# Performance work log

Hardware: AMD Instinct MI355X
Metric: run time of the kernel (lower is better)

The kernel has to match this reference:

```python
import jax, jax.numpy as jnp
import numpy as np

N_TRIPLES = 100_000    # number of (head, rel, attr) triples
TOTAL_CHARS = 1_600_000  # total characters across all attribute strings (~16/triple)
CHAR_VOCAB = 10_000
N_ENT = 100_000
D = 128                # embedding dim shared by char and entity tables


def setup_inputs() -> dict:
    key = jax.random.key(0)
    k1, k2, k3, k4, k5 = jax.random.split(key, 5)
    char_embeddings = jax.random.normal(k1, (CHAR_VOCAB, D), dtype=jnp.float32)
    entity_embeddings = jax.random.normal(k2, (N_ENT, D), dtype=jnp.float32)
    head_ids = jax.random.randint(k3, (N_TRIPLES,), 0, N_ENT, dtype=jnp.int32)
    char_ids = jax.random.randint(k4, (TOTAL_CHARS,), 0, CHAR_VOCAB, dtype=jnp.int32)
    # sorted segment ids emulate the per-triple ragged grouping (offsets form)
    segment_ids = jnp.sort(jax.random.randint(k5, (TOTAL_CHARS,), 0, N_TRIPLES, dtype=jnp.int32))
    return {
        "char_embeddings": char_embeddings,
        "entity_embeddings": entity_embeddings,
        "head_ids": head_ids,
        "char_ids": char_ids,
        "segment_ids": segment_ids,
    }


def reference(char_embeddings, entity_embeddings, head_ids, char_ids, segment_ids):
    n = head_ids.shape[0]
    # ragged embedding-bag: gather char rows, sum within each triple's segment
    t = jax.ops.segment_sum(char_embeddings[char_ids], segment_ids, num_segments=n)  # [N, D]
    h = entity_embeddings[head_ids]  # [N, D]
    # torch.norm with no dim = global Frobenius norm (faithful to original)
    h = h / jnp.linalg.norm(h)
    t = t / jnp.linalg.norm(t)
    return jnp.sum(1.0 - jnp.sum(h * t, axis=1))
```

## Files before the change

### kernel.cpp

```cpp
#include <hip/hip_runtime.h>

#define DIM   128
#define HALF  64
#define CPT   256
#define TAIL  64
#define WPB   4

__global__ __launch_bounds__(256) void fused_kernel(
    const float* __restrict__ char_emb,
    const float* __restrict__ ent,
    const int* __restrict__ head_ids,
    const int* __restrict__ char_ids,
    const int* __restrict__ seg_ids,
    float* __restrict__ pb,
    int total_chars, int n_triples, int hh_per_block)
{
    __shared__ __align__(16) int s_off[WPB][CPT + TAIL];
    __shared__ int s_sid[WPB][CPT + TAIL];
    __shared__ float r_scr[3][WPB];

    const int tid  = threadIdx.x;
    const int lane = tid & 63;
    const int wid  = tid >> 6;
    const int colb = lane << 2;

    float ht = 0.f, tt = 0.f, hh = 0.f;

    const int slice = blockIdx.x & 1;
    const int sco   = slice << 8;
    const int chunk = (blockIdx.x >> 1) * WPB + wid;
    const int start = chunk * CPT;
    const int len   = min(CPT, total_chars - start);
    const int sl    = min(CPT + TAIL, total_chars - start);
    const char* cb  = (const char*)char_emb;
    const float* ee = ent + slice * HALF + lane;

    for (int c = lane; c < sl; c += 64) {
        s_off[wid][c] = (char_ids[start + c] << 9) + sco;
        s_sid[wid][c] = seg_ids[start + c];
    }
    unsigned long long mk[4] = {0ull, 0ull, 0ull, 0ull};
    if (len == CPT) {
#pragma unroll
        for (int grp = 0; grp < 4; ++grp) {
            const int c = start + grp * 64 + lane;
            const int s1 = seg_ids[c];
            const int s0 = (c > 0) ? seg_ids[c - 1] : (s1 + 1);
            mk[grp] = __ballot(s1 != s0);
        }
    }
    __syncthreads();

    if (len == CPT) {
        int cur = __builtin_amdgcn_readfirstlane(s_sid[wid][0]);
        float hv = ee[(size_t)head_ids[cur] * DIM];
        float acc = 0.f;
        bool live = false;
        float vA[16], vB[16];

#define PF(BUF, B) { \
    _Pragma("unroll") \
    for (int q = 0; q < 4; ++q) { \
        const int4 o4 = *(const int4*)&s_off[wid][(B) * 16 + q * 4]; \
        BUF[q * 4 + 0] = *(const float*)(cb + (size_t)(unsigned)(o4.x + colb)); \
        BUF[q * 4 + 1] = *(const float*)(cb + (size_t)(unsigned)(o4.y + colb)); \
        BUF[q * 4 + 2] = *(const float*)(cb + (size_t)(unsigned)(o4.z + colb)); \
        BUF[q * 4 + 3] = *(const float*)(cb + (size_t)(unsigned)(o4.w + colb)); \
    } }

#define CS(BUF, B) { \
    _Pragma("unroll") \
    for (int j = 0; j < 16; ++j) { \
        if (mk[(B) >> 2] & (1ull << (((B) & 3) * 16 + j))) {    \
            if (live) { ht = fmaf(hv, acc, ht); tt = fmaf(acc, acc, tt); } \
            live = true; \
            acc = 0.f; \
            cur = __builtin_amdgcn_readfirstlane(s_sid[wid][(B) * 16 + j]); \
            hv = ee[(size_t)head_ids[cur] * DIM];     \
        } \
        acc += BUF[j]; \
    } }

        PF(vA, 0)
#pragma unroll
        for (int B = 0; B < 16; ++B) {
            if (B + 1 < 16) { if (B & 1) { PF(vA, B + 1) } else { PF(vB, B + 1) } }
            if (B & 1) { CS(vB, B) } else { CS(vA, B) }
        }

        if (live) {
            int e = CPT;
            bool ended = false;
            while (e < sl) {
                const int idx = e + lane;
                const bool differ = (idx < sl) && (s_sid[wid][idx] != cur);
                const unsigned long long bm = __ballot(differ);
                const int run = bm ? (__ffsll((long long)bm) - 1)
                                   : min(64, sl - e);
                for (int j = 0; j < run; j += 4) {
                    const int mm2 = min(4, run - j);
                    float vv[4];
#pragma unroll
                    for (int k = 0; k < 4; ++k) {
                        if (k < mm2)
                            vv[k] = *(const float*)(cb +
                                (size_t)(unsigned)(s_off[wid][e + j + k] + colb));
                    }
                    for (int k = 0; k < mm2; ++k) acc += vv[k];
                }
                e += run;
                if (bm) { ended = true; break; }
            }
            if (!ended && start + sl < total_chars) {
                int gg = start + sl;
                while (gg < total_chars && seg_ids[gg] == cur) {
                    acc += *(const float*)(cb +
                        (size_t)(unsigned)((char_ids[gg] << 9) + sco + colb));
                    ++gg;
                }
            }
            ht = fmaf(hv, acc, ht);
            tt = fmaf(acc, acc, tt);
        }
    } else if (len > 0) {
        const float* cembF = char_emb + slice * HALF + lane;
        int p = 0;
        if (start > 0) {
            const int prev = seg_ids[start - 1];
            while (p < len && seg_ids[start + p] == prev) ++p;
        }
        if (p < len) {
            int cur = seg_ids[start + p];
            float acc = 0.f;
            float hv = ee[(size_t)head_ids[cur] * DIM];
            for (int c = p; c < len; ++c) {
                const int sid = seg_ids[start + c];
                if (sid != cur) {
                    ht += hv * acc; tt += acc * acc;
                    acc = 0.f; cur = sid;
                    hv = ee[(size_t)head_ids[cur] * DIM];
                }
                acc += cembF[(size_t)char_ids[start + c] * DIM];
            }
            int gg = start + len;
            while (gg < total_chars && seg_ids[gg] == cur) {
                acc += cembF[(size_t)char_ids[gg] * DIM];
                ++gg;
            }
            ht += hv * acc; tt += acc * acc;
        }
    }

    {
        const float4* e4 = (const float4*)ent;
        const long base = (long)blockIdx.x * hh_per_block * 32;
        const long lim  = (long)n_triples * 32;
        for (int s = tid; s < hh_per_block * 32; s += 256) {
            const long f = base + s;
            if (f < lim) {
                const int row = (int)(f >> 5);
                const int hid = head_ids[row];
                const float4 v = e4[(size_t)hid * 32 + (int)(f & 31)];
                hh += v.x * v.x + v.y * v.y + v.z * v.z + v.w * v.w;
            }
        }
    }

#pragma unroll
    for (int off = 32; off > 0; off >>= 1) {
        ht += __shfl_down(ht, off);
        tt += __shfl_down(tt, off);
        hh += __shfl_down(hh, off);
    }
    if (lane == 0) { r_scr[0][wid] = ht; r_scr[1][wid] = tt; r_scr[2][wid] = hh; }
    __syncthreads();
    if (tid == 0) {
        float a = 0.f, b = 0.f, c = 0.f;
#pragma unroll
        for (int w = 0; w < WPB; ++w) {
            a += r_scr[0][w]; b += r_scr[1][w]; c += r_scr[2][w];
        }
        pb[blockIdx.x * 3 + 0] = a;
        pb[blockIdx.x * 3 + 1] = b;
        pb[blockIdx.x * 3 + 2] = c;
    }
}

__global__ __launch_bounds__(256) void reduce_kernel(
    const float* __restrict__ pb, int nb, float* __restrict__ out,
    int n_triples)
{
    double ht = 0.0, tt = 0.0, hh = 0.0;
    for (int i = threadIdx.x; i < nb; i += 256) {
        ht += (double)pb[i * 3 + 0];
        tt += (double)pb[i * 3 + 1];
        hh += (double)pb[i * 3 + 2];
    }
#pragma unroll
    for (int off = 32; off > 0; off >>= 1) {
        ht += __shfl_down(ht, off);
        tt += __shfl_down(tt, off);
        hh += __shfl_down(hh, off);
    }
    __shared__ double sd[3][4];
    const int wid = threadIdx.x >> 6;
    if ((threadIdx.x & 63) == 0) { sd[0][wid] = ht; sd[1][wid] = tt; sd[2][wid] = hh; }
    __syncthreads();
    if (threadIdx.x == 0) {
        double a = 0.0, b = 0.0, c = 0.0;
        for (int w = 0; w < 4; ++w) { a += sd[0][w]; b += sd[1][w]; c += sd[2][w]; }
        out[0] = (float)((double)n_triples - a / sqrt(c * b));
    }
}

extern "C" void kernel_launch(void* const* d_in, const int* in_sizes, int n_in,
                              void* d_out, int out_size, void* d_ws, size_t ws_size,
                              hipStream_t stream)
{
    const float* char_emb = (const float*)d_in[0];
    const float* ent_emb  = (const float*)d_in[1];
    const int* head_ids   = (const int*)d_in[2];
    const int* char_ids   = (const int*)d_in[3];
    const int* seg_ids    = (const int*)d_in[4];
    const int n_triples   = in_sizes[2];
    const int total_chars = in_sizes[3];

    const int n_chunks = (total_chars + CPT - 1) / CPT;
    const int bps = (n_chunks + WPB - 1) / WPB;
    const int nsb = 2 * bps;
    const int hhpb = (n_triples + nsb - 1) / nsb;

    float* pb = (float*)d_ws;

    fused_kernel<<<nsb, 256, 0, stream>>>(char_emb, ent_emb, head_ids,
                                          char_ids, seg_ids, pb,
                                          total_chars, n_triples, hhpb);
    reduce_kernel<<<1, 256, 0, stream>>>(pb, nsb, (float*)d_out, n_triples);
}
```

Before: 165.4 us.

## Process full embedding row per wave with float2 loads and prefetched head ids

```diff
diff --git a/kernel.cpp b/kernel.cpp
--- a/kernel.cpp
+++ b/kernel.cpp
@@ -1,10 +1,10 @@
 #include <hip/hip_runtime.h>
 
 #define DIM   128
-#define HALF  64
 #define CPT   256
 #define TAIL  64
 #define WPB   4
+#define QD    40
 
 __global__ __launch_bounds__(256) void fused_kernel(
     const float* __restrict__ char_emb,
@@ -17,68 +17,83 @@
 {
     __shared__ __align__(16) int s_off[WPB][CPT + TAIL];
     __shared__ int s_sid[WPB][CPT + TAIL];
+    __shared__ int s_hq[WPB][QD];
     __shared__ float r_scr[3][WPB];
 
     const int tid  = threadIdx.x;
     const int lane = tid & 63;
     const int wid  = tid >> 6;
-    const int colb = lane << 2;
+    const int colb = lane << 3;
 
     float ht = 0.f, tt = 0.f, hh = 0.f;
 
-    const int slice = blockIdx.x & 1;
-    const int sco   = slice << 8;
-    const int chunk = (blockIdx.x >> 1) * WPB + wid;
+    const int chunk = blockIdx.x * WPB + wid;
     const int start = chunk * CPT;
     const int len   = min(CPT, total_chars - start);
     const int sl    = min(CPT + TAIL, total_chars - start);
     const char* cb  = (const char*)char_emb;
-    const float* ee = ent + slice * HALF + lane;
+    const float* ee = ent + (lane << 1);
 
     for (int c = lane; c < sl; c += 64) {
-        s_off[wid][c] = (char_ids[start + c] << 9) + sco;
+        s_off[wid][c] = char_ids[start + c] << 9;
         s_sid[wid][c] = seg_ids[start + c];
     }
+
     unsigned long long mk[4] = {0ull, 0ull, 0ull, 0ull};
     if (len == CPT) {
+        int rbase = 0;
 #pragma unroll
         for (int grp = 0; grp < 4; ++grp) {
-            const int c = start + grp * 64 + lane;
-            const int s1 = seg_ids[c];
-            const int s0 = (c > 0) ? seg_ids[c - 1] : (s1 + 1);
-            mk[grp] = __ballot(s1 != s0);
+            const int cc = grp * 64 + lane;
+            const int s1 = s_sid[wid][cc];
+            const int ip = (cc > 0) ? cc - 1 : 0;
+            int s0 = s_sid[wid][ip];
+            if (cc == 0) s0 = (start > 0) ? seg_ids[start - 1] : s1 + 1;
+            const bool bnd = (s1 != s0);
+            mk[grp] = __ballot(bnd);
+            const int rk = rbase + (int)__popcll(mk[grp] & ((1ull << lane) - 1ull));
+            if (bnd && rk < QD) s_hq[wid][rk] = head_ids[s1];
+            rbase += (int)__popcll(mk[grp]);
         }
     }
     __syncthreads();
 
     if (len == CPT) {
-        int cur = __builtin_amdgcn_readfirstlane(s_sid[wid][0]);
-        float hv = ee[(size_t)head_ids[cur] * DIM];
-        float acc = 0.f;
+        int cur = 0;
+        float2 hv;  hv.x = 0.f;  hv.y = 0.f;
+        float2 acc; acc.x = 0.f; acc.y = 0.f;
         bool live = false;
-        float vA[16], vB[16];
+        int rk = 0;
+        int nhid = __builtin_amdgcn_readfirstlane(s_hq[wid][0]);
+        float2 vA[16], vB[16];
 
 #define PF(BUF, B) { \
     _Pragma("unroll") \
     for (int q = 0; q < 4; ++q) { \
         const int4 o4 = *(const int4*)&s_off[wid][(B) * 16 + q * 4]; \
-        BUF[q * 4 + 0] = *(const float*)(cb + (size_t)(unsigned)(o4.x + colb)); \
-        BUF[q * 4 + 1] = *(const float*)(cb + (size_t)(unsigned)(o4.y + colb)); \
-        BUF[q * 4 + 2] = *(const float*)(cb + (size_t)(unsigned)(o4.z + colb)); \
-        BUF[q * 4 + 3] = *(const float*)(cb + (size_t)(unsigned)(o4.w + colb)); \
+        BUF[q * 4 + 0] = *(const float2*)(cb + (size_t)(unsigned)(o4.x + colb)); \
+        BUF[q * 4 + 1] = *(const float2*)(cb + (size_t)(unsigned)(o4.y + colb)); \
+        BUF[q * 4 + 2] = *(const float2*)(cb + (size_t)(unsigned)(o4.z + colb)); \
+        BUF[q * 4 + 3] = *(const float2*)(cb + (size_t)(unsigned)(o4.w + colb)); \
     } }
 
 #define CS(BUF, B) { \
     _Pragma("unroll") \
     for (int j = 0; j < 16; ++j) { \
         if (mk[(B) >> 2] & (1ull << (((B) & 3) * 16 + j))) {    \
-            if (live) { ht = fmaf(hv, acc, ht); tt = fmaf(acc, acc, tt); } \
+            if (live) { \
+                ht = fmaf(hv.x, acc.x, ht); ht = fmaf(hv.y, acc.y, ht); \
+                tt = fmaf(acc.x, acc.x, tt); tt = fmaf(acc.y, acc.y, tt); \
+            } \
             live = true; \
-            acc = 0.f; \
+            acc.x = 0.f; acc.y = 0.f; \
             cur = __builtin_amdgcn_readfirstlane(s_sid[wid][(B) * 16 + j]); \
-            hv = ee[(size_t)head_ids[cur] * DIM];     \
+            const int hid = (rk < QD) ? nhid : head_ids[cur];   \
+            hv = *(const float2*)(ee + (size_t)hid * DIM); \
+            ++rk; \
+            nhid = __builtin_amdgcn_readfirstlane(s_hq[wid][rk < QD ? rk : QD - 1]); \
         } \
-        acc += BUF[j]; \
+        acc.x += BUF[j].x; acc.y += BUF[j].y; \
     } }
 
         PF(vA, 0)
@@ -99,14 +114,14 @@
                                    : min(64, sl - e);
                 for (int j = 0; j < run; j += 4) {
                     const int mm2 = min(4, run - j);
-                    float vv[4];
+                    float2 vv[4];
 #pragma unroll
                     for (int k = 0; k < 4; ++k) {
                         if (k < mm2)
-                            vv[k] = *(const float*)(cb +
+                            vv[k] = *(const float2*)(cb +
                                 (size_t)(unsigned)(s_off[wid][e + j + k] + colb));
                     }
-                    for (int k = 0; k < mm2; ++k) acc += vv[k];
+                    for (int k = 0; k < mm2; ++k) { acc.x += vv[k].x; acc.y += vv[k].y; }
                 }
                 e += run;
                 if (bm) { ended = true; break; }
@@ -114,40 +129,46 @@
             if (!ended && start + sl < total_chars) {
                 int gg = start + sl;
                 while (gg < total_chars && seg_ids[gg] == cur) {
-                    acc += *(const float*)(cb +
-                        (size_t)(unsigned)((char_ids[gg] << 9) + sco + colb));
+                    const float2 v = *(const float2*)(cb +
+                        (size_t)(unsigned)((char_ids[gg] << 9) + colb));
+                    acc.x += v.x; acc.y += v.y;
                     ++gg;
                 }
             }
-            ht = fmaf(hv, acc, ht);
-            tt = fmaf(acc, acc, tt);
+            ht = fmaf(hv.x, acc.x, ht); ht = fmaf(hv.y, acc.y, ht);
+            tt = fmaf(acc.x, acc.x, tt); tt = fmaf(acc.y, acc.y, tt);
         }
     } else if (len > 0) {
-        const float* cembF = char_emb + slice * HALF + lane;
         int p = 0;
         if (start > 0) {
             const int prev = seg_ids[start - 1];
             while (p < len && seg_ids[start + p] == prev) ++p;
         }
         if (p < len) {
-            int cur = seg_ids[start + p];
-            float acc = 0.f;
-            float hv = ee[(size_t)head_ids[cur] * DIM];
+            int cur2 = seg_ids[start + p];
+            float2 acc; acc.x = 0.f; acc.y = 0.f;
+            float2 hv = *(const float2*)(ee + (size_t)head_ids[cur2] * DIM);
             for (int c = p; c < len; ++c) {
                 const int sid = seg_ids[start + c];
-                if (sid != cur) {
-                    ht += hv * acc; tt += acc * acc;
-                    acc = 0.f; cur = sid;
-                    hv = ee[(size_t)head_ids[cur] * DIM];
+                if (sid != cur2) {
+                    ht += hv.x * acc.x + hv.y * acc.y;
+                    tt += acc.x * acc.x + acc.y * acc.y;
+                    acc.x = 0.f; acc.y = 0.f; cur2 = sid;
+                    hv = *(const float2*)(ee + (size_t)head_ids[cur2] * DIM);
                 }
-                acc += cembF[(size_t)char_ids[start + c] * DIM];
+                const float2 v = *(const float2*)(cb +
+                    (size_t)(unsigned)((char_ids[start + c] << 9) + colb));
+                acc.x += v.x; acc.y += v.y;
             }
             int gg = start + len;
-            while (gg < total_chars && seg_ids[gg] == cur) {
-                acc += cembF[(size_t)char_ids[gg] * DIM];
+            while (gg < total_chars && seg_ids[gg] == cur2) {
+                const float2 v = *(const float2*)(cb +
+                    (size_t)(unsigned)((char_ids[gg] << 9) + colb));
+                acc.x += v.x; acc.y += v.y;
                 ++gg;
             }
-            ht += hv * acc; tt += acc * acc;
+            ht += hv.x * acc.x + hv.y * acc.y;
+            tt += acc.x * acc.x + acc.y * acc.y;
         }
     }
 
@@ -226,8 +247,7 @@
     const int total_chars = in_sizes[3];
 
     const int n_chunks = (total_chars + CPT - 1) / CPT;
-    const int bps = (n_chunks + WPB - 1) / WPB;
-    const int nsb = 2 * bps;
+    const int nsb = (n_chunks + WPB - 1) / WPB;
     const int hhpb = (n_triples + nsb - 1) / nsb;
 
     float* pb = (float*)d_ws;
```

Result: slower. 188.4 us (+13.9%).

## Reuse gathered head rows for hh norm and prefetch them into LDS

Applied to the files above, without the earlier changes.

```diff
diff --git a/kernel.cpp b/kernel.cpp
--- a/kernel.cpp
+++ b/kernel.cpp
@@ -5,6 +5,7 @@
 #define CPT   256
 #define TAIL  64
 #define WPB   4
+#define QD    24
 
 __global__ __launch_bounds__(256) void fused_kernel(
     const float* __restrict__ char_emb,
@@ -13,10 +14,12 @@
     const int* __restrict__ char_ids,
     const int* __restrict__ seg_ids,
     float* __restrict__ pb,
-    int total_chars, int n_triples, int hh_per_block)
+    int total_chars, int n_triples)
 {
     __shared__ __align__(16) int s_off[WPB][CPT + TAIL];
     __shared__ int s_sid[WPB][CPT + TAIL];
+    __shared__ __align__(16) int s_hq[WPB][QD];
+    __shared__ float s_hv[WPB][QD][64];
     __shared__ float r_scr[3][WPB];
 
     const int tid  = threadIdx.x;
@@ -39,23 +42,59 @@
         s_off[wid][c] = (char_ids[start + c] << 9) + sco;
         s_sid[wid][c] = seg_ids[start + c];
     }
+
     unsigned long long mk[4] = {0ull, 0ull, 0ull, 0ull};
+    int nbq = 0;
     if (len == CPT) {
+        int rbase = 0;
 #pragma unroll
         for (int grp = 0; grp < 4; ++grp) {
             const int c = start + grp * 64 + lane;
             const int s1 = seg_ids[c];
             const int s0 = (c > 0) ? seg_ids[c - 1] : (s1 + 1);
-            mk[grp] = __ballot(s1 != s0);
+            const bool bnd = (s1 != s0);
+            mk[grp] = __ballot(bnd);
+            const int rk = rbase + (int)__popcll(mk[grp] & ((1ull << lane) - 1ull));
+            if (bnd && rk < QD) s_hq[wid][rk] = head_ids[s1];
+            rbase += (int)__popcll(mk[grp]);
+        }
+        nbq = min(rbase, QD);
+
+        int r = 0;
+        for (; r + 4 <= nbq; r += 4) {
+            const int4 q4 = *(const int4*)&s_hq[wid][r];
+            const int h0 = __builtin_amdgcn_readfirstlane(q4.x);
+            const int h1 = __builtin_amdgcn_readfirstlane(q4.y);
+            const int h2 = __builtin_amdgcn_readfirstlane(q4.z);
+            const int h3 = __builtin_amdgcn_readfirstlane(q4.w);
+            const float v0 = ee[(size_t)h0 * DIM];
+            const float v1 = ee[(size_t)h1 * DIM];
+            const float v2 = ee[(size_t)h2 * DIM];
+            const float v3 = ee[(size_t)h3 * DIM];
+            hh = fmaf(v0, v0, hh); hh = fmaf(v1, v1, hh);
+            hh = fmaf(v2, v2, hh); hh = fmaf(v3, v3, hh);
+            s_hv[wid][r + 0][lane] = v0;
+            s_hv[wid][r + 1][lane] = v1;
+            s_hv[wid][r + 2][lane] = v2;
+            s_hv[wid][r + 3][lane] = v3;
+        }
+        for (; r < nbq; ++r) {
+            const int h0 = __builtin_amdgcn_readfirstlane(s_hq[wid][r]);
+            const float v0 = ee[(size_t)h0 * DIM];
+            hh = fmaf(v0, v0, hh);
+            s_hv[wid][r][lane] = v0;
         }
     }
     __syncthreads();
 
     if (len == CPT) {
-        int cur = __builtin_amdgcn_readfirstlane(s_sid[wid][0]);
-        float hv = ee[(size_t)head_ids[cur] * DIM];
+        int cur = (start > 0) ? seg_ids[start - 1]
+                              : __builtin_amdgcn_readfirstlane(s_sid[wid][0]);
+        float hv = 0.f;
+        float pv = s_hv[wid][0][lane];
         float acc = 0.f;
         bool live = false;
+        int rk = 0;
         float vA[16], vB[16];
 
 #define PF(BUF, B) { \
@@ -75,8 +114,23 @@
             if (live) { ht = fmaf(hv, acc, ht); tt = fmaf(acc, acc, tt); } \
             live = true; \
             acc = 0.f; \
-            cur = __builtin_amdgcn_readfirstlane(s_sid[wid][(B) * 16 + j]); \
-            hv = ee[(size_t)head_ids[cur] * DIM];     \
+            const int news = __builtin_amdgcn_readfirstlane(s_sid[wid][(B) * 16 + j]); \
+            if (news > cur + 1) {                \
+                for (int g = cur + 1; g < news; ++g) { \
+                    const float gv = ee[(size_t)head_ids[g] * DIM]; \
+                    hh = fmaf(gv, gv, hh); \
+                } \
+            } \
+            cur = news; \
+            if (rk < QD) {                       \
+                hv = pv; \
+                const int nxt = (rk + 1 < QD) ? rk + 1 : QD - 1; \
+                pv = s_hv[wid][nxt][lane]; \
+            } else {                             \
+                hv = ee[(size_t)head_ids[cur] * DIM]; \
+                hh = fmaf(hv, hv, hh); \
+            } \
+            ++rk; \
         } \
         acc += BUF[j]; \
     } }
@@ -130,39 +184,36 @@
             while (p < len && seg_ids[start + p] == prev) ++p;
         }
         if (p < len) {
-            int cur = seg_ids[start + p];
+            int cur2 = seg_ids[start + p];
+            if (start > 0) {
+                for (int g = seg_ids[start - 1] + 1; g < cur2; ++g) {
+                    const float gv = ee[(size_t)head_ids[g] * DIM];
+                    hh = fmaf(gv, gv, hh);
+                }
+            }
             float acc = 0.f;
-            float hv = ee[(size_t)head_ids[cur] * DIM];
+            float hv = ee[(size_t)head_ids[cur2] * DIM];
+            hh = fmaf(hv, hv, hh);
             for (int c = p; c < len; ++c) {
                 const int sid = seg_ids[start + c];
-                if (sid != cur) {
+                if (sid != cur2) {
                     ht += hv * acc; tt += acc * acc;
-                    acc = 0.f; cur = sid;
-                    hv = ee[(size_t)head_ids[cur] * DIM];
+                    for (int g = cur2 + 1; g < sid; ++g) {
+                        const float gv = ee[(size_t)head_ids[g] * DIM];
+                        hh = fmaf(gv, gv, hh);
+                    }
+                    acc = 0.f; cur2 = sid;
+                    hv = ee[(size_t)head_ids[cur2] * DIM];
+                    hh = fmaf(hv, hv, hh);
                 }
                 acc += cembF[(size_t)char_ids[start + c] * DIM];
             }
             int gg = start + len;
-            while (gg < total_chars && seg_ids[gg] == cur) {
+            while (gg < total_chars && seg_ids[gg] == cur2) {
                 acc += cembF[(size_t)char_ids[gg] * DIM];
                 ++gg;
             }
             ht += hv * acc; tt += acc * acc;
-        }
-    }
-
-    {
-        const float4* e4 = (const float4*)ent;
-        const long base = (long)blockIdx.x * hh_per_block * 32;
-        const long lim  = (long)n_triples * 32;
-        for (int s = tid; s < hh_per_block * 32; s += 256) {
-            const long f = base + s;
-            if (f < lim) {
-                const int row = (int)(f >> 5);
-                const int hid = head_ids[row];
-                const float4 v = e4[(size_t)hid * 32 + (int)(f & 31)];
-                hh += v.x * v.x + v.y * v.y + v.z * v.z + v.w * v.w;
-            }
         }
     }
 
@@ -188,13 +239,28 @@
 
 __global__ __launch_bounds__(256) void reduce_kernel(
     const float* __restrict__ pb, int nb, float* __restrict__ out,
-    int n_triples)
+    int n_triples, const int* __restrict__ seg_ids,
+    const int* __restrict__ head_ids, const float* __restrict__ ent,
+    int total_chars)
 {
     double ht = 0.0, tt = 0.0, hh = 0.0;
     for (int i = threadIdx.x; i < nb; i += 256) {
         ht += (double)pb[i * 3 + 0];
         tt += (double)pb[i * 3 + 1];
         hh += (double)pb[i * 3 + 2];
+    }
+    int first = n_triples, last = n_triples - 1;
+    if (total_chars > 0) { first = seg_ids[0]; last = seg_ids[total_chars - 1]; }
+    const int lead  = first;
+    const int trail = n_triples - 1 - last;
+    const int tot   = lead + trail;
+    const float4* e4 = (const float4*)ent;
+    for (int w = threadIdx.x; w < tot * 32; w += 256) {
+        const int rr = w >> 5;
+        const int g  = (rr < lead) ? rr : (last + 1 + (rr - lead));
+        const float4 v = e4[(size_t)head_ids[g] * 32 + (w & 31)];
+        hh += (double)v.x * v.x + (double)v.y * v.y
+            + (double)v.z * v.z + (double)v.w * v.w;
     }
 #pragma unroll
     for (int off = 32; off > 0; off >>= 1) {
@@ -227,13 +293,14 @@
 
     const int n_chunks = (total_chars + CPT - 1) / CPT;
     const int bps = (n_chunks + WPB - 1) / WPB;
-    const int nsb = 2 * bps;
-    const int hhpb = (n_triples + nsb - 1) / nsb;
+    const int nsb = (2 * bps > 0) ? 2 * bps : 2;
 
     float* pb = (float*)d_ws;
 
     fused_kernel<<<nsb, 256, 0, stream>>>(char_emb, ent_emb, head_ids,
                                           char_ids, seg_ids, pb,
-                                          total_chars, n_triples, hhpb);
-    reduce_kernel<<<1, 256, 0, stream>>>(pb, nsb, (float*)d_out, n_triples);
+                                          total_chars, n_triples);
+    reduce_kernel<<<1, 256, 0, stream>>>(pb, nsb, (float*)d_out, n_triples,
+                                         seg_ids, head_ids, ent_emb,
+                                         total_chars);
 }
```

Result: slower. 186.7 us (+12.8%).

## Precompute per-segment head ids in LDS and deepen char-row prefetch to three buffers

Applied to the files above, without the earlier changes.

```diff
diff --git a/kernel.cpp b/kernel.cpp
--- a/kernel.cpp
+++ b/kernel.cpp
@@ -5,6 +5,7 @@
 #define CPT   256
 #define TAIL  64
 #define WPB   4
+#define QD    32
 
 __global__ __launch_bounds__(256) void fused_kernel(
     const float* __restrict__ char_emb,
@@ -17,6 +18,7 @@
 {
     __shared__ __align__(16) int s_off[WPB][CPT + TAIL];
     __shared__ int s_sid[WPB][CPT + TAIL];
+    __shared__ int s_hq[WPB][QD];
     __shared__ float r_scr[3][WPB];
 
     const int tid  = threadIdx.x;
@@ -41,22 +43,28 @@
     }
     unsigned long long mk[4] = {0ull, 0ull, 0ull, 0ull};
     if (len == CPT) {
+        int rbase = 0;
 #pragma unroll
         for (int grp = 0; grp < 4; ++grp) {
             const int c = start + grp * 64 + lane;
             const int s1 = seg_ids[c];
             const int s0 = (c > 0) ? seg_ids[c - 1] : (s1 + 1);
-            mk[grp] = __ballot(s1 != s0);
+            const bool bnd = (s1 != s0);
+            mk[grp] = __ballot(bnd);
+            const int rk0 = rbase + (int)__popcll(mk[grp] & ((1ull << lane) - 1ull));
+            if (bnd && rk0 < QD) s_hq[wid][rk0] = head_ids[s1];
+            rbase += (int)__popcll(mk[grp]);
         }
     }
     __syncthreads();
 
     if (len == CPT) {
-        int cur = __builtin_amdgcn_readfirstlane(s_sid[wid][0]);
-        float hv = ee[(size_t)head_ids[cur] * DIM];
+        float hv = 0.f;
         float acc = 0.f;
         bool live = false;
-        float vA[16], vB[16];
+        int rk = 0;
+        int nhid = s_hq[wid][0];
+        float vA[16], vB[16], vC[16];
 
 #define PF(BUF, B) { \
     _Pragma("unroll") \
@@ -75,20 +83,37 @@
             if (live) { ht = fmaf(hv, acc, ht); tt = fmaf(acc, acc, tt); } \
             live = true; \
             acc = 0.f; \
-            cur = __builtin_amdgcn_readfirstlane(s_sid[wid][(B) * 16 + j]); \
-            hv = ee[(size_t)head_ids[cur] * DIM];     \
+            int hid_; \
+            if (rk < QD) {                       \
+                hid_ = nhid; \
+            } else {                             \
+                const int cs_ = __builtin_amdgcn_readfirstlane(s_sid[wid][(B) * 16 + j]); \
+                hid_ = head_ids[cs_]; \
+            } \
+            ++rk; \
+            nhid = s_hq[wid][rk < QD ? rk : (QD - 1)]; \
+            hv = ee[(size_t)(unsigned)hid_ * DIM];    \
         } \
         acc += BUF[j]; \
     } }
 
         PF(vA, 0)
+        PF(vB, 1)
 #pragma unroll
         for (int B = 0; B < 16; ++B) {
-            if (B + 1 < 16) { if (B & 1) { PF(vA, B + 1) } else { PF(vB, B + 1) } }
-            if (B & 1) { CS(vB, B) } else { CS(vA, B) }
+            const int nb2 = B + 2;
+            if (nb2 < 16) {
+                if (nb2 % 3 == 0)      { PF(vA, nb2) }
+                else if (nb2 % 3 == 1) { PF(vB, nb2) }
+                else                   { PF(vC, nb2) }
+            }
+            if (B % 3 == 0)      { CS(vA, B) }
+            else if (B % 3 == 1) { CS(vB, B) }
+            else                 { CS(vC, B) }
         }
 
         if (live) {
+            int cur = __builtin_amdgcn_readfirstlane(s_sid[wid][CPT - 1]);
             int e = CPT;
             bool ended = false;
             while (e < sl) {
```

Result: slower. 178.2 us (+7.7%).
